# Optimization experiments

Hardware: AMD Instinct MI355X
Metric: run time of the kernel (lower is better)

## Reference

```python
import jax, jax.numpy as jnp
import numpy as np

N_SRC = 50000   # source nodes in the block
N_DST = 50000   # destination nodes
E = 800000      # edges (avg in-degree 16, every dst has >=1 edge)
D = 256         # hidden_dim
V = 50000       # vocab_size
C = 104         # n_classes (POJ-104)


def setup_inputs() -> dict:
    key = jax.random.key(0)
    k1, k2, k3, k4, k5, k6 = jax.random.split(key, 6)
    token_id = jax.random.randint(k1, (N_SRC,), 0, V, dtype=jnp.int32)
    src_idx = jax.random.randint(k2, (E,), 0, N_SRC, dtype=jnp.int32)
    # every dst node gets at least one in-edge (DGL raises on 0-in-degree),
    # remaining edges land on random dst nodes; sorted so edges are grouped by dst
    extra = jax.random.randint(k3, (E - N_DST,), 0, N_DST, dtype=jnp.int32)
    dst_idx = jnp.sort(jnp.concatenate([jnp.arange(N_DST, dtype=jnp.int32), extra]))
    emb = jax.random.normal(k4, (V, D), dtype=jnp.float32)  # nn.Embedding default N(0,1)
    W = jax.random.normal(k5, (D, D), dtype=jnp.float32) / jnp.sqrt(D)
    b = jnp.zeros((D,), dtype=jnp.float32)
    Wc = jax.random.normal(k6, (C, D), dtype=jnp.float32) / jnp.sqrt(D)
    bc = jnp.zeros((C,), dtype=jnp.float32)
    return {"emb": emb, "W": W, "b": b, "Wc": Wc, "bc": bc,
            "token_id": token_id, "src_idx": src_idx, "dst_idx": dst_idx}


def reference(emb, W, b, Wc, bc, token_id, src_idx, dst_idx):
    # embedding gather for source nodes (first_layer branch)
    feat_src = emb[token_id]                  # [N_SRC, D]
    # message: copy_u -> mailbox messages per edge
    msgs = feat_src[src_idx]                  # [E, D]
    # per-dst segment stats (dst_idx is sorted / grouped by dst)
    deg = jax.ops.segment_sum(jnp.ones((E,), dtype=jnp.int32), dst_idx,
                              num_segments=N_DST)            # [N_DST]
    sum_all = jax.ops.segment_sum(msgs, dst_idx, num_segments=N_DST)  # [N_DST, D]
    # DGL mailbox reducer: last message in the segment is the 'current input',
    # the rest are children summed through CodeRNNCell: x = cur + relu(W @ sum_children + b)
    last_idx = jnp.cumsum(deg) - 1            # index of last edge per dst segment
    last_msg = msgs[last_idx]                 # [N_DST, D]
    child_sum = sum_all - last_msg            # sum of msgs excluding the last one
    rnn_out = last_msg + jax.nn.relu(child_sum @ W.T + b)
    # length == 1 segments bypass the RNN cell entirely: ft = the single message
    ft = jnp.where((deg == 1)[:, None], last_msg, rnn_out)   # [N_DST, D]
    # final classifier
    return ft @ Wc.T + bc                     # [N_DST, C]
```

## Files before the change

kernel.cpp:

```cpp
#include <hip/hip_runtime.h>
#include <hip/hip_bf16.h>

#define DD 256
#define CC 104

typedef __bf16 bf16x8 __attribute__((ext_vector_type(8)));
typedef float  f32x4  __attribute__((ext_vector_type(4)));

__device__ inline float bu2f(unsigned short u) {
    return __uint_as_float(((unsigned)u) << 16);
}
__device__ inline unsigned short f2bu(float f) {
    __hip_bfloat16 h = __float2bfloat16(f);
    return *reinterpret_cast<unsigned short*>(&h);
}

__global__ void prep_convert_kernel(
    const int* __restrict__ token_id,
    const int* __restrict__ src_idx,
    const int* __restrict__ dst_idx,
    int* __restrict__ seg_start,
    int* __restrict__ seg_end,
    int* __restrict__ edge_tok,
    int E, int prep_blocks,
    const float* __restrict__ emb,
    const float* __restrict__ W,
    const float* __restrict__ Wc,
    __hip_bfloat16* __restrict__ embb,
    __hip_bfloat16* __restrict__ Wb,
    __hip_bfloat16* __restrict__ Wcb,
    int nE4)
{
    if ((int)blockIdx.x < prep_blocks) {
        int e = blockIdx.x * blockDim.x + threadIdx.x;
        if (e >= E) return;
        int d = dst_idx[e];
        edge_tok[e] = token_id[src_idx[e]];
        if (e == 0 || dst_idx[e - 1] != d) seg_start[d] = e;
        if (e == E - 1 || dst_idx[e + 1] != d) seg_end[d] = e + 1;
        return;
    }
    const int nW4  = DD * DD / 4;
    const int nWc4 = 128 * DD / 4;
    int i = (blockIdx.x - prep_blocks) * blockDim.x + threadIdx.x;
    float4 v;
    __hip_bfloat16* dst;
    if (i < nE4) {
        v = ((const float4*)emb)[i];
        dst = embb + (size_t)i * 4;
    } else if (i < nE4 + nW4) {
        int j = i - nE4;
        v = ((const float4*)W)[j];
        dst = Wb + (size_t)j * 4;
    } else if (i < nE4 + nW4 + nWc4) {
        int j = i - nE4 - nW4;
        v = (j < CC * DD / 4) ? ((const float4*)Wc)[j]
                              : make_float4(0.f, 0.f, 0.f, 0.f);
        dst = Wcb + (size_t)j * 4;
    } else return;
    ushort4 o;
    o.x = f2bu(v.x); o.y = f2bu(v.y); o.z = f2bu(v.z); o.w = f2bu(v.w);
    *(ushort4*)dst = o;
}

__global__ void seg_sum_kernel(const __hip_bfloat16* __restrict__ embb,
                               const int* __restrict__ edge_tok,
                               const int* __restrict__ seg_start,
                               const int* __restrict__ seg_end,
                               __hip_bfloat16* __restrict__ childb,
                               int n_dst)
{
    int w = (blockIdx.x * blockDim.x + threadIdx.x) >> 6;
    int lane = threadIdx.x & 63;
    if (w >= n_dst) return;
    int h   = lane >> 5;
    int l32 = lane & 31;
    int s = seg_start[w];
    int e = seg_end[w] - 1;
    float acc[8] = {0.f,0.f,0.f,0.f,0.f,0.f,0.f,0.f};

    auto accum = [&](int tok) {
        uint4 u = *(const uint4*)(embb + (size_t)tok * DD + l32 * 8);
        const unsigned* ud = (const unsigned*)&u;
#pragma unroll
        for (int d = 0; d < 4; ++d) {
            acc[2*d]   += __uint_as_float(ud[d] << 16);
            acc[2*d+1] += __uint_as_float(ud[d] & 0xffff0000u);
        }
    };

    int i = s + h;
    for (; i + 2 < e; i += 4) {
        int t0 = edge_tok[i];
        int t1 = edge_tok[i + 2];
        uint4 u0 = *(const uint4*)(embb + (size_t)t0 * DD + l32 * 8);
        uint4 u1 = *(const uint4*)(embb + (size_t)t1 * DD + l32 * 8);
        const unsigned* a0 = (const unsigned*)&u0;
        const unsigned* a1 = (const unsigned*)&u1;
#pragma unroll
        for (int d = 0; d < 4; ++d) {
            acc[2*d]   += __uint_as_float(a0[d] << 16) + __uint_as_float(a1[d] << 16);
            acc[2*d+1] += __uint_as_float(a0[d] & 0xffff0000u) + __uint_as_float(a1[d] & 0xffff0000u);
        }
    }
    if (i < e) accum(edge_tok[i]);

#pragma unroll
    for (int j = 0; j < 8; ++j) acc[j] += __shfl_xor(acc[j], 32, 64);

    if (h == 0) {
        uint4 o;
        unsigned* od = (unsigned*)&o;
#pragma unroll
        for (int d = 0; d < 4; ++d)
            od[d] = (unsigned)f2bu(acc[2*d]) | ((unsigned)f2bu(acc[2*d+1]) << 16);
        *(uint4*)(childb + (size_t)w * DD + l32 * 8) = o;
    }
}

__global__ __launch_bounds__(256, 2) void rnn_mfma(
    __hip_bfloat16* childft,
    const __hip_bfloat16* __restrict__ Wb,
    const float* __restrict__ bvec,
    const __hip_bfloat16* __restrict__ embb,
    const int* __restrict__ seg_start,
    const int* __restrict__ seg_end,
    const int* __restrict__ edge_tok,
    int M)
{
    extern __shared__ char smem[];
    __hip_bfloat16* lds = (__hip_bfloat16*)smem;
    const int t    = threadIdx.x;
    const int lane = t & 63;
    const int wid  = t >> 6;
    const int quad = lane >> 4;
    const int l16  = lane & 15;
    const int mw   = blockIdx.x * 128 + wid * 32;

    int  mrow[2], ltok[2];
    bool multi[2];
    bf16x8 cfrag[2][8];
#pragma unroll
    for (int mt = 0; mt < 2; ++mt) {
        mrow[mt] = min(mw + mt * 16 + l16, M - 1);
        int ls = seg_start[mrow[mt]];
        int le = seg_end[mrow[mt]];
        multi[mt] = (le - ls) > 1;
        ltok[mt]  = edge_tok[le - 1];
        const __hip_bfloat16* arow = childft + (size_t)mrow[mt] * DD + quad * 8;
#pragma unroll
        for (int k0 = 0; k0 < 8; ++k0)
            cfrag[mt][k0] = *(const bf16x8*)(arow + k0 * 32);
    }

    f32x4 acc[2][16];
#pragma unroll
    for (int mt = 0; mt < 2; ++mt)
#pragma unroll
        for (int nt = 0; nt < 16; ++nt) acc[mt][nt] = (f32x4){0.f,0.f,0.f,0.f};

    for (int p = 0; p < 2; ++p) {
        if (p) __syncthreads();
#pragma unroll
        for (int it = 0; it < 16; ++it) {
            int idx = it * 256 + t;
            int g = idx >> 6, s = idx & 63;
            int nt = g & 15, kl = g >> 4;
            int row = nt * 16 + (s & 15);
            int col = (p * 4 + kl) * 32 + (s >> 4) * 8;
            *(bf16x8*)(lds + g * 512 + s * 8) =
                *(const bf16x8*)(Wb + (size_t)row * DD + col);
        }
        __syncthreads();
#pragma unroll
        for (int kl = 0; kl < 4; ++kl) {
#pragma unroll
            for (int nt = 0; nt < 16; ++nt) {
                bf16x8 wf = *(const bf16x8*)(lds + (kl * 16 + nt) * 512 + lane * 8);
                acc[0][nt] = __builtin_amdgcn_mfma_f32_16x16x32_bf16(wf, cfrag[0][p*4+kl], acc[0][nt], 0, 0, 0);
                acc[1][nt] = __builtin_amdgcn_mfma_f32_16x16x32_bf16(wf, cfrag[1][p*4+kl], acc[1][nt], 0, 0, 0);
            }
        }
    }

#pragma unroll
    for (int mt = 0; mt < 2; ++mt) {
        int m = mw + mt * 16 + l16;
        if (m < M) {
            const __hip_bfloat16* lrow = embb + (size_t)ltok[mt] * DD;
            bool mu = multi[mt];
#pragma unroll
            for (int nt = 0; nt < 16; ++nt) {
                int c0 = nt * 16 + quad * 4;
                float4 bia = *(const float4*)(bvec + c0);
                ushort4 lm = *(const ushort4*)(lrow + c0);
                ushort4 o;
                float v0 = mu ? fmaxf(acc[mt][nt][0] + bia.x, 0.f) : 0.f;
                float v1 = mu ? fmaxf(acc[mt][nt][1] + bia.y, 0.f) : 0.f;
                float v2 = mu ? fmaxf(acc[mt][nt][2] + bia.z, 0.f) : 0.f;
                float v3 = mu ? fmaxf(acc[mt][nt][3] + bia.w, 0.f) : 0.f;
                o.x = f2bu(v0 + bu2f(lm.x));
                o.y = f2bu(v1 + bu2f(lm.y));
                o.z = f2bu(v2 + bu2f(lm.z));
                o.w = f2bu(v3 + bu2f(lm.w));
                *(ushort4*)(childft + (size_t)m * DD + c0) = o;
            }
        }
    }
}

__global__ __launch_bounds__(256, 2) void cls_mfma(
    const __hip_bfloat16* __restrict__ ftb,
    const __hip_bfloat16* __restrict__ Wcb,
    const float* __restrict__ bc,
    float* __restrict__ out,
    int M)
{
    extern __shared__ char smem[];
    __hip_bfloat16* lds = (__hip_bfloat16*)smem;
    const int t    = threadIdx.x;
    const int lane = t & 63;
    const int wid  = t >> 6;
    const int quad = lane >> 4;
    const int l16  = lane & 15;
    const int mw   = blockIdx.x * 128 + wid * 32;

    int mrow[2];
    bf16x8 ffrag[2][8];
#pragma unroll
    for (int mt = 0; mt < 2; ++mt) {
        mrow[mt] = min(mw + mt * 16 + l16, M - 1);
        const __hip_bfloat16* arow = ftb + (size_t)mrow[mt] * DD + quad * 8;
#pragma unroll
        for (int k0 = 0; k0 < 8; ++k0)
            ffrag[mt][k0] = *(const bf16x8*)(arow + k0 * 32);
    }

#pragma unroll
    for (int it = 0; it < 16; ++it) {
        int idx = it * 256 + t;
        int g = idx >> 6, s = idx & 63;
        int nt = g & 7, k0 = g >> 3;
        int row = nt * 16 + (s & 15);
        int col = k0 * 32 + (s >> 4) * 8;
        *(bf16x8*)(lds + g * 512 + s * 8) =
            *(const bf16x8*)(Wcb + (size_t)row * DD + col);
    }
    __syncthreads();

    f32x4 acc[2][8];
#pragma unroll
    for (int mt = 0; mt < 2; ++mt)
#pragma unroll
        for (int nt = 0; nt < 8; ++nt) acc[mt][nt] = (f32x4){0.f,0.f,0.f,0.f};

#pragma unroll
    for (int k0 = 0; k0 < 8; ++k0) {
#pragma unroll
        for (int nt = 0; nt < 8; ++nt) {
            bf16x8 wf = *(const bf16x8*)(lds + (k0 * 8 + nt) * 512 + lane * 8);
            acc[0][nt] = __builtin_amdgcn_mfma_f32_16x16x32_bf16(wf, ffrag[0][k0], acc[0][nt], 0, 0, 0);
            acc[1][nt] = __builtin_amdgcn_mfma_f32_16x16x32_bf16(wf, ffrag[1][k0], acc[1][nt], 0, 0, 0);
        }
    }

#pragma unroll
    for (int mt = 0; mt < 2; ++mt) {
        int m = mw + mt * 16 + l16;
        if (m < M) {
#pragma unroll
            for (int nt = 0; nt < 8; ++nt) {
                int c0 = nt * 16 + quad * 4;
                if (c0 <= 100) {
                    float4 bia = *(const float4*)(bc + c0);
                    float4 o;
                    o.x = acc[mt][nt][0] + bia.x;
                    o.y = acc[mt][nt][1] + bia.y;
                    o.z = acc[mt][nt][2] + bia.z;
                    o.w = acc[mt][nt][3] + bia.w;
                    *(float4*)(out + (size_t)m * CC + c0) = o;
                }
            }
        }
    }
}

extern "C" void kernel_launch(void* const* d_in, const int* in_sizes, int n_in,
                              void* d_out, int out_size, void* d_ws, size_t ws_size,
                              hipStream_t stream)
{
    const float* emb      = (const float*)d_in[0];
    const float* W        = (const float*)d_in[1];
    const float* bvec     = (const float*)d_in[2];
    const float* Wc       = (const float*)d_in[3];
    const float* bc       = (const float*)d_in[4];
    const int*   token_id = (const int*)d_in[5];
    const int*   src_idx  = (const int*)d_in[6];
    const int*   dst_idx  = (const int*)d_in[7];
    float*       out      = (float*)d_out;

    const int E     = in_sizes[6];
    const int Vemb  = in_sizes[0] / DD;
    const int n_dst = out_size / CC;
    (void)n_in; (void)ws_size;

    char* ws = (char*)d_ws;
    size_t off = 0;
    auto alloc = [&](size_t bytes) {
        void* p = ws + off;
        off = (off + bytes + 255) & ~(size_t)255;
        return p;
    };
    int* seg_start = (int*)alloc((size_t)n_dst * sizeof(int));
    int* seg_end   = (int*)alloc((size_t)n_dst * sizeof(int));
    int* edge_tok  = (int*)alloc((size_t)E * sizeof(int));
    __hip_bfloat16* childb = (__hip_bfloat16*)alloc((size_t)n_dst * DD * 2);
    __hip_bfloat16* embb   = (__hip_bfloat16*)alloc((size_t)Vemb * DD * 2);
    __hip_bfloat16* Wb     = (__hip_bfloat16*)alloc((size_t)DD * DD * 2);
    __hip_bfloat16* Wcb    = (__hip_bfloat16*)alloc((size_t)128 * DD * 2);

    const int nE4 = Vemb * (DD / 4);
    const int cvt_total   = nE4 + DD * DD / 4 + 128 * DD / 4;
    const int prep_blocks = (E + 255) / 256;
    const int cvt_blocks  = (cvt_total + 255) / 256;
    const int gemm_blocks = (n_dst + 127) / 128;

    prep_convert_kernel<<<prep_blocks + cvt_blocks, 256, 0, stream>>>(
        token_id, src_idx, dst_idx, seg_start, seg_end, edge_tok, E,
        prep_blocks, emb, W, Wc, embb, Wb, Wcb, nE4);
    seg_sum_kernel<<<(n_dst + 3) / 4, 256, 0, stream>>>(
        embb, edge_tok, seg_start, seg_end, childb, n_dst);
    rnn_mfma<<<gemm_blocks, 256, 65536, stream>>>(
        childb, Wb, bvec, embb, seg_start, seg_end, edge_tok, n_dst);
    cls_mfma<<<gemm_blocks, 256, 65536, stream>>>(
        childb, Wcb, bc, out, n_dst);
}
```

Before: 199.7 us.

## Split RNN GEMM over N, shrink classifier tiles, deepen gather unroll

```diff
diff --git a/kernel.cpp b/kernel.cpp
--- a/kernel.cpp
+++ b/kernel.cpp
@@ -79,31 +79,38 @@
     int e = seg_end[w] - 1;
     float acc[8] = {0.f,0.f,0.f,0.f,0.f,0.f,0.f,0.f};
 
-    auto accum = [&](int tok) {
-        uint4 u = *(const uint4*)(embb + (size_t)tok * DD + l32 * 8);
+    int i = s + h;
+    for (; i + 6 < e; i += 8) {
+        int t0 = edge_tok[i];
+        int t1 = edge_tok[i + 2];
+        int t2 = edge_tok[i + 4];
+        int t3 = edge_tok[i + 6];
+        uint4 u0 = *(const uint4*)(embb + (size_t)t0 * DD + l32 * 8);
+        uint4 u1 = *(const uint4*)(embb + (size_t)t1 * DD + l32 * 8);
+        uint4 u2 = *(const uint4*)(embb + (size_t)t2 * DD + l32 * 8);
+        uint4 u3 = *(const uint4*)(embb + (size_t)t3 * DD + l32 * 8);
+        const unsigned* a0 = (const unsigned*)&u0;
+        const unsigned* a1 = (const unsigned*)&u1;
+        const unsigned* a2 = (const unsigned*)&u2;
+        const unsigned* a3 = (const unsigned*)&u3;
+#pragma unroll
+        for (int d = 0; d < 4; ++d) {
+            acc[2*d]   += (__uint_as_float(a0[d] << 16) + __uint_as_float(a1[d] << 16))
+                        + (__uint_as_float(a2[d] << 16) + __uint_as_float(a3[d] << 16));
+            acc[2*d+1] += (__uint_as_float(a0[d] & 0xffff0000u) + __uint_as_float(a1[d] & 0xffff0000u))
+                        + (__uint_as_float(a2[d] & 0xffff0000u) + __uint_as_float(a3[d] & 0xffff0000u));
+        }
+    }
+    for (; i < e; i += 2) {
+        int t0 = edge_tok[i];
+        uint4 u = *(const uint4*)(embb + (size_t)t0 * DD + l32 * 8);
         const unsigned* ud = (const unsigned*)&u;
 #pragma unroll
         for (int d = 0; d < 4; ++d) {
             acc[2*d]   += __uint_as_float(ud[d] << 16);
             acc[2*d+1] += __uint_as_float(ud[d] & 0xffff0000u);
         }
-    };
-
-    int i = s + h;
-    for (; i + 2 < e; i += 4) {
-        int t0 = edge_tok[i];
-        int t1 = edge_tok[i + 2];
-        uint4 u0 = *(const uint4*)(embb + (size_t)t0 * DD + l32 * 8);
-        uint4 u1 = *(const uint4*)(embb + (size_t)t1 * DD + l32 * 8);
-        const unsigned* a0 = (const unsigned*)&u0;
-        const unsigned* a1 = (const unsigned*)&u1;
-#pragma unroll
-        for (int d = 0; d < 4; ++d) {
-            acc[2*d]   += __uint_as_float(a0[d] << 16) + __uint_as_float(a1[d] << 16);
-            acc[2*d+1] += __uint_as_float(a0[d] & 0xffff0000u) + __uint_as_float(a1[d] & 0xffff0000u);
-        }
-    }
-    if (i < e) accum(edge_tok[i]);
+    }
 
 #pragma unroll
     for (int j = 0; j < 8; ++j) acc[j] += __shfl_xor(acc[j], 32, 64);
@@ -118,8 +125,9 @@
     }
 }
 
-__global__ __launch_bounds__(256, 2) void rnn_mfma(
-    __hip_bfloat16* childft,
+__global__ __launch_bounds__(256, 3) void rnn_mfma(
+    const __hip_bfloat16* __restrict__ childb,
+    __hip_bfloat16* __restrict__ ftb,
     const __hip_bfloat16* __restrict__ Wb,
     const float* __restrict__ bvec,
     const __hip_bfloat16* __restrict__ embb,
@@ -130,12 +138,13 @@
 {
     extern __shared__ char smem[];
     __hip_bfloat16* lds = (__hip_bfloat16*)smem;
-    const int t    = threadIdx.x;
-    const int lane = t & 63;
-    const int wid  = t >> 6;
-    const int quad = lane >> 4;
-    const int l16  = lane & 15;
-    const int mw   = blockIdx.x * 128 + wid * 32;
+    const int t     = threadIdx.x;
+    const int lane  = t & 63;
+    const int wid   = t >> 6;
+    const int quad  = lane >> 4;
+    const int l16   = lane & 15;
+    const int mw    = blockIdx.x * 128 + wid * 32;
+    const int nbase = blockIdx.y * 8;
 
     int  mrow[2], ltok[2];
     bool multi[2];
@@ -147,26 +156,26 @@
         int le = seg_end[mrow[mt]];
         multi[mt] = (le - ls) > 1;
         ltok[mt]  = edge_tok[le - 1];
-        const __hip_bfloat16* arow = childft + (size_t)mrow[mt] * DD + quad * 8;
+        const __hip_bfloat16* arow = childb + (size_t)mrow[mt] * DD + quad * 8;
 #pragma unroll
         for (int k0 = 0; k0 < 8; ++k0)
             cfrag[mt][k0] = *(const bf16x8*)(arow + k0 * 32);
     }
 
-    f32x4 acc[2][16];
+    f32x4 acc[2][8];
 #pragma unroll
     for (int mt = 0; mt < 2; ++mt)
 #pragma unroll
-        for (int nt = 0; nt < 16; ++nt) acc[mt][nt] = (f32x4){0.f,0.f,0.f,0.f};
+        for (int nt = 0; nt < 8; ++nt) acc[mt][nt] = (f32x4){0.f,0.f,0.f,0.f};
 
     for (int p = 0; p < 2; ++p) {
         if (p) __syncthreads();
 #pragma unroll
-        for (int it = 0; it < 16; ++it) {
+        for (int it = 0; it < 8; ++it) {
             int idx = it * 256 + t;
             int g = idx >> 6, s = idx & 63;
-            int nt = g & 15, kl = g >> 4;
-            int row = nt * 16 + (s & 15);
+            int ntl = g & 7, kl = g >> 3;
+            int row = (nbase + ntl) * 16 + (s & 15);
             int col = (p * 4 + kl) * 32 + (s >> 4) * 8;
             *(bf16x8*)(lds + g * 512 + s * 8) =
                 *(const bf16x8*)(Wb + (size_t)row * DD + col);
@@ -174,11 +183,12 @@
         __syncthreads();
 #pragma unroll
         for (int kl = 0; kl < 4; ++kl) {
-#pragma unroll
-            for (int nt = 0; nt < 16; ++nt) {
-                bf16x8 wf = *(const bf16x8*)(lds + (kl * 16 + nt) * 512 + lane * 8);
-                acc[0][nt] = __builtin_amdgcn_mfma_f32_16x16x32_bf16(wf, cfrag[0][p*4+kl], acc[0][nt], 0, 0, 0);
-                acc[1][nt] = __builtin_amdgcn_mfma_f32_16x16x32_bf16(wf, cfrag[1][p*4+kl], acc[1][nt], 0, 0, 0);
+            int k0 = p * 4 + kl;
+#pragma unroll
+            for (int nt = 0; nt < 8; ++nt) {
+                bf16x8 wf = *(const bf16x8*)(lds + (kl * 8 + nt) * 512 + lane * 8);
+                acc[0][nt] = __builtin_amdgcn_mfma_f32_16x16x32_bf16(wf, cfrag[0][k0], acc[0][nt], 0, 0, 0);
+                acc[1][nt] = __builtin_amdgcn_mfma_f32_16x16x32_bf16(wf, cfrag[1][k0], acc[1][nt], 0, 0, 0);
             }
         }
     }
@@ -190,8 +200,8 @@
             const __hip_bfloat16* lrow = embb + (size_t)ltok[mt] * DD;
             bool mu = multi[mt];
 #pragma unroll
-            for (int nt = 0; nt < 16; ++nt) {
-                int c0 = nt * 16 + quad * 4;
+            for (int nt = 0; nt < 8; ++nt) {
+                int c0 = (nbase + nt) * 16 + quad * 4;
                 float4 bia = *(const float4*)(bvec + c0);
                 ushort4 lm = *(const ushort4*)(lrow + c0);
                 ushort4 o;
@@ -203,13 +213,13 @@
                 o.y = f2bu(v1 + bu2f(lm.y));
                 o.z = f2bu(v2 + bu2f(lm.z));
                 o.w = f2bu(v3 + bu2f(lm.w));
-                *(ushort4*)(childft + (size_t)m * DD + c0) = o;
+                *(ushort4*)(ftb + (size_t)m * DD + c0) = o;
             }
         }
     }
 }
 
-__global__ __launch_bounds__(256, 2) void cls_mfma(
+__global__ __launch_bounds__(256, 4) void cls_mfma(
     const __hip_bfloat16* __restrict__ ftb,
     const __hip_bfloat16* __restrict__ Wcb,
     const float* __restrict__ bc,
@@ -223,63 +233,56 @@
     const int wid  = t >> 6;
     const int quad = lane >> 4;
     const int l16  = lane & 15;
-    const int mw   = blockIdx.x * 128 + wid * 32;
-
-    int mrow[2];
-    bf16x8 ffrag[2][8];
-#pragma unroll
-    for (int mt = 0; mt < 2; ++mt) {
-        mrow[mt] = min(mw + mt * 16 + l16, M - 1);
-        const __hip_bfloat16* arow = ftb + (size_t)mrow[mt] * DD + quad * 8;
-#pragma unroll
-        for (int k0 = 0; k0 < 8; ++k0)
-            ffrag[mt][k0] = *(const bf16x8*)(arow + k0 * 32);
-    }
-
-#pragma unroll
-    for (int it = 0; it < 16; ++it) {
-        int idx = it * 256 + t;
-        int g = idx >> 6, s = idx & 63;
-        int nt = g & 7, k0 = g >> 3;
-        int row = nt * 16 + (s & 15);
-        int col = k0 * 32 + (s >> 4) * 8;
-        *(bf16x8*)(lds + g * 512 + s * 8) =
-            *(const bf16x8*)(Wcb + (size_t)row * DD + col);
-    }
-    __syncthreads();
-
-    f32x4 acc[2][8];
-#pragma unroll
-    for (int mt = 0; mt < 2; ++mt)
-#pragma unroll
-        for (int nt = 0; nt < 8; ++nt) acc[mt][nt] = (f32x4){0.f,0.f,0.f,0.f};
-
-#pragma unroll
-    for (int k0 = 0; k0 < 8; ++k0) {
+    const int mw   = blockIdx.x * 64 + wid * 16;
+
+    int mrow = min(mw + l16, M - 1);
+    bf16x8 ffrag[8];
+    const __hip_bfloat16* arow = ftb + (size_t)mrow * DD + quad * 8;
+#pragma unroll
+    for (int k0 = 0; k0 < 8; ++k0)
+        ffrag[k0] = *(const bf16x8*)(arow + k0 * 32);
+
+    f32x4 acc[8];
+#pragma unroll
+    for (int nt = 0; nt < 8; ++nt) acc[nt] = (f32x4){0.f,0.f,0.f,0.f};
+
+    for (int p = 0; p < 2; ++p) {
+        if (p) __syncthreads();
+#pragma unroll
+        for (int it = 0; it < 8; ++it) {
+            int idx = it * 256 + t;
+            int g = idx >> 6, s = idx & 63;
+            int nt = g & 7, kl = g >> 3;
+            int row = nt * 16 + (s & 15);
+            int col = (p * 4 + kl) * 32 + (s >> 4) * 8;
+            *(bf16x8*)(lds + g * 512 + s * 8) =
+                *(const bf16x8*)(Wcb + (size_t)row * DD + col);
+        }
+        __syncthreads();
+#pragma unroll
+        for (int kl = 0; kl < 4; ++kl) {
+            int k0 = p * 4 + kl;
+#pragma unroll
+            for (int nt = 0; nt < 8; ++nt) {
+                bf16x8 wf = *(const bf16x8*)(lds + (kl * 8 + nt) * 512 + lane * 8);
+                acc[nt] = __builtin_amdgcn_mfma_f32_16x16x32_bf16(wf, ffrag[k0], acc[nt], 0, 0, 0);
+            }
+        }
+    }
+
+    int m = mw + l16;
+    if (m < M) {
 #pragma unroll
         for (int nt = 0; nt < 8; ++nt) {
-            bf16x8 wf = *(const bf16x8*)(lds + (k0 * 8 + nt) * 512 + lane * 8);
-            acc[0][nt] = __builtin_amdgcn_mfma_f32_16x16x32_bf16(wf, ffrag[0][k0], acc[0][nt], 0, 0, 0);
-            acc[1][nt] = __builtin_amdgcn_mfma_f32_16x16x32_bf16(wf, ffrag[1][k0], acc[1][nt], 0, 0, 0);
-        }
-    }
-
-#pragma unroll
-    for (int mt = 0; mt < 2; ++mt) {
-        int m = mw + mt * 16 + l16;
-        if (m < M) {
-#pragma unroll
-            for (int nt = 0; nt < 8; ++nt) {
-                int c0 = nt * 16 + quad * 4;
-                if (c0 <= 100) {
-                    float4 bia = *(const float4*)(bc + c0);
-                    float4 o;
-                    o.x = acc[mt][nt][0] + bia.x;
-                    o.y = acc[mt][nt][1] + bia.y;
-                    o.z = acc[mt][nt][2] + bia.z;
-                    o.w = acc[mt][nt][3] + bia.w;
-                    *(float4*)(out + (size_t)m * CC + c0) = o;
-                }
+            int c0 = nt * 16 + quad * 4;
+            if (c0 <= 100) {
+                float4 bia = *(const float4*)(bc + c0);
+                float4 o;
+                o.x = acc[nt][0] + bia.x;
+                o.y = acc[nt][1] + bia.y;
+                o.z = acc[nt][2] + bia.z;
+                o.w = acc[nt][3] + bia.w;
+                *(float4*)(out + (size_t)m * CC + c0) = o;
             }
         }
     }
@@ -315,6 +318,7 @@
     int* seg_end   = (int*)alloc((size_t)n_dst * sizeof(int));
     int* edge_tok  = (int*)alloc((size_t)E * sizeof(int));
     __hip_bfloat16* childb = (__hip_bfloat16*)alloc((size_t)n_dst * DD * 2);
+    __hip_bfloat16* ftb    = (__hip_bfloat16*)alloc((size_t)n_dst * DD * 2);
     __hip_bfloat16* embb   = (__hip_bfloat16*)alloc((size_t)Vemb * DD * 2);
     __hip_bfloat16* Wb     = (__hip_bfloat16*)alloc((size_t)DD * DD * 2);
     __hip_bfloat16* Wcb    = (__hip_bfloat16*)alloc((size_t)128 * DD * 2);
@@ -323,15 +327,16 @@
     const int cvt_total   = nE4 + DD * DD / 4 + 128 * DD / 4;
     const int prep_blocks = (E + 255) / 256;
     const int cvt_blocks  = (cvt_total + 255) / 256;
-    const int gemm_blocks = (n_dst + 127) / 128;
+    const int rnn_strips  = (n_dst + 127) / 128;
+    const int cls_blocks  = (n_dst + 63) / 64;
 
     prep_convert_kernel<<<prep_blocks + cvt_blocks, 256, 0, stream>>>(
         token_id, src_idx, dst_idx, seg_start, seg_end, edge_tok, E,
         prep_blocks, emb, W, Wc, embb, Wb, Wcb, nE4);
     seg_sum_kernel<<<(n_dst + 3) / 4, 256, 0, stream>>>(
         embb, edge_tok, seg_start, seg_end, childb, n_dst);
-    rnn_mfma<<<gemm_blocks, 256, 65536, stream>>>(
-        childb, Wb, bvec, embb, seg_start, seg_end, edge_tok, n_dst);
-    cls_mfma<<<gemm_blocks, 256, 65536, stream>>>(
-        childb, Wcb, bc, out, n_dst);
-}
+    rnn_mfma<<<dim3(rnn_strips, 2), 256, 32768, stream>>>(
+        childb, ftb, Wb, bvec, embb, seg_start, seg_end, edge_tok, n_dst);
+    cls_mfma<<<cls_blocks, 256, 32768, stream>>>(
+        ftb, Wcb, bc, out, n_dst);
+}
```

Result: slower. 206.3 us (+3.3%).
